# Performance work log

Hardware: AMD Instinct MI355X
Metric: run time of the kernel (lower is better)

The kernel has to match this reference:

```python
import jax, jax.numpy as jnp
import numpy as np


def _pairwise_l2(x, y):
    # x: [N, D], y: [M, D] -> [N, M] Euclidean distances, computed via the
    # intermediate the original torch code materializes).
    x2 = jnp.sum(x * x, axis=-1)                      # [N]
    y2 = jnp.sum(y * y, axis=-1)                      # [M]
    xy = x @ y.T                                      # [N, M]
    d2 = jnp.maximum(x2[:, None] + y2[None, :] - 2.0 * xy, 0.0)
    return jnp.sqrt(d2)


def setup_inputs() -> dict:
    key = jax.random.key(0)
    k1, k2 = jax.random.split(key)
    pred = jax.random.normal(k1, (8192, 3), dtype=jnp.float32)
    label = jax.random.normal(k2, (8192, 3), dtype=jnp.float32)
    return {"pred": pred, "label": label}


def reference(pred, label):
    dis = _pairwise_l2(pred, label)                   # [N, M]
    dis_xy = jnp.mean(jnp.min(dis, axis=1))           # mean over x of nearest y
    dis_yx = jnp.mean(jnp.min(dis, axis=0))           # mean over y of nearest x
    return dis_xy + dis_yx
```

## Files before the change

### kernel.cpp

```cpp
#include <hip/hip_runtime.h>

constexpr int N    = 8192;
constexpr int BLK  = 256;
constexpr int BX   = 128;
constexpr int BY   = 1024;
constexpr int NYR  = N / BY;
constexpr int P    = 8;
constexpr int NSL  = 16;
constexpr int SY   = BY / NSL;
constexpr int SPAD = SY + 1;
constexpr int RPAD = BX + 4;

__global__ __launch_bounds__(BLK) void chamfer_stage1(
    const float* __restrict__ pred, const float* __restrict__ label,
    float* __restrict__ minbuf)
{
    int b   = blockIdx.x;
    int dir = b >> 9;
    int xbk = (b >> 3) & 63;
    int yr  = b & 7;

    const float* A = dir ? label : pred;
    const float* B = dir ? pred  : label;

    __shared__ float4 sy[NSL * SPAD];
    __shared__ float  red[NSL * RPAD];

    int u  = threadIdx.x & 15;
    int ys = threadIdx.x >> 4;

    float xa[P], xb[P], xc[P], nx[P], m[P];
    #pragma unroll
    for (int k = 0; k < P; ++k) {
        int idx = xbk * BX + k * 16 + u;
        float a = A[3*idx], c = A[3*idx+1], d = A[3*idx+2];
        xa[k] = -2.f * a;  xb[k] = -2.f * c;  xc[k] = -2.f * d;
        nx[k] = a*a + c*c + d*d;
        m[k]  = 3.4e38f;
    }

    for (int i = threadIdx.x; i < BY; i += BLK) {
        int g = yr * BY + i;
        float a = B[3*g], c = B[3*g+1], d = B[3*g+2];
        sy[(i / SY) * SPAD + (i & (SY-1))] = make_float4(a, c, d, a*a + c*c + d*d);
    }
    __syncthreads();

    const float4* s = &sy[ys * SPAD];
    #pragma unroll 4
    for (int j = 0; j < SY; j += 2) {
        float4 ya = s[j], yb = s[j + 1];
        #pragma unroll
        for (int k = 0; k < P; ++k) {
            float sa = fmaf(xa[k], ya.x, fmaf(xb[k], ya.y, fmaf(xc[k], ya.z, ya.w)));
            float sb = fmaf(xa[k], yb.x, fmaf(xb[k], yb.y, fmaf(xc[k], yb.z, yb.w)));
            m[k] = fminf(fminf(sa, sb), m[k]);
        }
    }

    #pragma unroll
    for (int k = 0; k < P; ++k)
        red[ys * RPAD + k * 16 + u] = fmaxf(m[k] + nx[k], 0.f);
    __syncthreads();

    if (threadIdx.x < BX) {
        float v = red[threadIdx.x];
        #pragma unroll
        for (int q = 1; q < NSL; ++q)
            v = fminf(v, red[q * RPAD + threadIdx.x]);
        minbuf[yr * (2 * N) + dir * N + xbk * BX + threadIdx.x] = v;
    }
}

__global__ __launch_bounds__(1024) void chamfer_stage2(
    const float4* __restrict__ minbuf4, float* __restrict__ out)
{
    float s = 0.f;
    #pragma unroll
    for (int j = 0; j < (2 * N / 4) / 1024; ++j) {
        int g = j * 1024 + threadIdx.x;
        float4 v = minbuf4[g];
        #pragma unroll
        for (int r = 1; r < NYR; ++r) {
            float4 w = minbuf4[r * 4096 + g];
            v.x = fminf(v.x, w.x); v.y = fminf(v.y, w.y);
            v.z = fminf(v.z, w.z); v.w = fminf(v.w, w.w);
        }
        s += sqrtf(v.x) + sqrtf(v.y) + sqrtf(v.z) + sqrtf(v.w);
    }
    s *= (1.0f / N);
    for (int off = 32; off; off >>= 1) s += __shfl_down(s, off);
    __shared__ float r2[16];
    if ((threadIdx.x & 63) == 0) r2[threadIdx.x >> 6] = s;
    __syncthreads();
    if (threadIdx.x == 0) {
        float v = 0.f;
        #pragma unroll
        for (int i = 0; i < 16; ++i) v += r2[i];
        out[0] = v;
    }
}

extern "C" void kernel_launch(void* const* d_in, const int* in_sizes, int n_in,
                              void* d_out, int out_size, void* d_ws, size_t ws_size,
                              hipStream_t stream) {
    const float* pred  = (const float*)d_in[0];
    const float* label = (const float*)d_in[1];
    float* out    = (float*)d_out;
    float* minbuf = (float*)d_ws;

    chamfer_stage1<<<dim3(2 * (N / BX) * NYR), dim3(BLK),  0, stream>>>(pred, label, minbuf);
    chamfer_stage2<<<dim3(1), dim3(1024), 0, stream>>>((const float4*)minbuf, out);
}
```

Baseline: 24.20 us.

## Double the y-tile per block and spread the final reduction across blocks

Raises the y-chunk per stage-1 block from 1024 to 2048 points, halving the number of blocks (512 instead of 1024) and the partial-min buffer that stage 2 has to combine. Stage 2 becomes 16 blocks of 256 threads that each min-combine and sum a slice, and a new third kernel adds the 16 block sums. The goal is to cut the serial single-block reduction and the partial-buffer traffic. In exchange it adds a kernel launch, leaves fewer blocks to fill the GPU's compute units in stage 1, and gives each block more work.

```diff
diff --git a/kernel.cpp b/kernel.cpp
--- a/kernel.cpp
+++ b/kernel.cpp
@@ -3,7 +3,7 @@
 constexpr int N    = 8192;
 constexpr int BLK  = 256;
 constexpr int BX   = 128;
-constexpr int BY   = 1024;
+constexpr int BY   = 2048;
 constexpr int NYR  = N / BY;
 constexpr int P    = 8;
 constexpr int NSL  = 16;
@@ -16,9 +16,9 @@
     float* __restrict__ minbuf)
 {
     int b   = blockIdx.x;
-    int dir = b >> 9;
-    int xbk = (b >> 3) & 63;
-    int yr  = b & 7;
+    int dir = b >> 8;
+    int xbk = (b >> 2) & 63;
+    int yr  = b & 3;
 
     const float* A = dir ? label : pred;
     const float* B = dir ? pred  : label;
@@ -42,7 +42,7 @@
     for (int i = threadIdx.x; i < BY; i += BLK) {
         int g = yr * BY + i;
         float a = B[3*g], c = B[3*g+1], d = B[3*g+2];
-        sy[(i / SY) * SPAD + (i & (SY-1))] = make_float4(a, c, d, a*a + c*c + d*d);
+        sy[(i >> 7) * SPAD + (i & (SY-1))] = make_float4(a, c, d, a*a + c*c + d*d);
     }
     __syncthreads();
 
@@ -72,33 +72,32 @@
     }
 }
 
-__global__ __launch_bounds__(1024) void chamfer_stage2(
-    const float4* __restrict__ minbuf4, float* __restrict__ out)
+__global__ __launch_bounds__(256) void chamfer_stage2(
+    const float4* __restrict__ minbuf4, float* __restrict__ bsum)
 {
-    float s = 0.f;
+    int g = blockIdx.x * 256 + threadIdx.x;
+    float4 v = minbuf4[g];
     #pragma unroll
-    for (int j = 0; j < (2 * N / 4) / 1024; ++j) {
-        int g = j * 1024 + threadIdx.x;
-        float4 v = minbuf4[g];
-        #pragma unroll
-        for (int r = 1; r < NYR; ++r) {
-            float4 w = minbuf4[r * 4096 + g];
-            v.x = fminf(v.x, w.x); v.y = fminf(v.y, w.y);
-            v.z = fminf(v.z, w.z); v.w = fminf(v.w, w.w);
-        }
-        s += sqrtf(v.x) + sqrtf(v.y) + sqrtf(v.z) + sqrtf(v.w);
+    for (int r = 1; r < NYR; ++r) {
+        float4 w = minbuf4[r * 4096 + g];
+        v.x = fminf(v.x, w.x); v.y = fminf(v.y, w.y);
+        v.z = fminf(v.z, w.z); v.w = fminf(v.w, w.w);
     }
-    s *= (1.0f / N);
+    float s = sqrtf(v.x) + sqrtf(v.y) + sqrtf(v.z) + sqrtf(v.w);
     for (int off = 32; off; off >>= 1) s += __shfl_down(s, off);
-    __shared__ float r2[16];
+    __shared__ float r2[4];
     if ((threadIdx.x & 63) == 0) r2[threadIdx.x >> 6] = s;
     __syncthreads();
-    if (threadIdx.x == 0) {
-        float v = 0.f;
-        #pragma unroll
-        for (int i = 0; i < 16; ++i) v += r2[i];
-        out[0] = v;
-    }
+    if (threadIdx.x == 0)
+        bsum[blockIdx.x] = r2[0] + r2[1] + r2[2] + r2[3];
+}
+
+__global__ __launch_bounds__(64) void chamfer_stage3(
+    const float* __restrict__ bsum, float* __restrict__ out)
+{
+    float s = (threadIdx.x < 16) ? bsum[threadIdx.x] : 0.f;
+    for (int off = 32; off; off >>= 1) s += __shfl_down(s, off);
+    if (threadIdx.x == 0) out[0] = s * (1.0f / N);
 }
 
 extern "C" void kernel_launch(void* const* d_in, const int* in_sizes, int n_in,
@@ -108,7 +107,9 @@
     const float* label = (const float*)d_in[1];
     float* out    = (float*)d_out;
     float* minbuf = (float*)d_ws;
+    float* bsum   = minbuf + NYR * 2 * N;
 
-    chamfer_stage1<<<dim3(2 * (N / BX) * NYR), dim3(BLK),  0, stream>>>(pred, label, minbuf);
-    chamfer_stage2<<<dim3(1), dim3(1024), 0, stream>>>((const float4*)minbuf, out);
+    chamfer_stage1<<<dim3(2 * (N / BX) * NYR), dim3(BLK), 0, stream>>>(pred, label, minbuf);
+    chamfer_stage2<<<dim3(16), dim3(256), 0, stream>>>((const float4*)minbuf, bsum);
+    chamfer_stage3<<<dim3(1), dim3(64), 0, stream>>>(bsum, out);
 }
```

Measured after the change: 19.69 us. 1.23x faster.
